# Kernel tuning notes

Measured on AMD Instinct MI355X. Metric: run time of the kernel, lower is better.

## Reference

```python
import jax, jax.numpy as jnp
import numpy as np

NUM_HEADS = 16
HEAD_DIM = 128
EMBED_DIM = 2048
BASE = 10000.0


def rope(x, offset=0):
    # x: [b, h, n, d]  rotary positional embedding (lrpe_type=1)
    d = x.shape[-1]
    n = x.shape[-2]
    inv_freq = 1.0 / (BASE ** (jnp.arange(0, d, 2, dtype=jnp.float32) / d))  # [d/2]
    pos = jnp.arange(n, dtype=jnp.float32) + offset                          # [n]
    ang = pos[:, None] * inv_freq[None, :]                                   # [n, d/2]
    cos, sin = jnp.cos(ang), jnp.sin(ang)
    x1, x2 = x[..., 0::2], x[..., 1::2]
    out1 = x1 * cos - x2 * sin
    out2 = x1 * sin + x2 * cos
    return jnp.stack([out1, out2], axis=-1).reshape(x.shape)


def setup_inputs() -> dict:
    key = jax.random.key(0)
    ks = jax.random.split(key, 5)
    b, n = 2, 2048
    std = 0.02
    x = jax.random.normal(ks[0], (b, n, EMBED_DIM), dtype=jnp.float32)
    Wq = jax.random.normal(ks[1], (NUM_HEADS * HEAD_DIM, EMBED_DIM), dtype=jnp.float32) * std
    Wkv = jax.random.normal(ks[2], (2 * HEAD_DIM, EMBED_DIM), dtype=jnp.float32) * std
    Wkvh = jax.random.normal(ks[3], (2 * NUM_HEADS, EMBED_DIM), dtype=jnp.float32) * std
    Wo = jax.random.normal(ks[4], (EMBED_DIM, NUM_HEADS * HEAD_DIM), dtype=jnp.float32) * std
    return {"x": x, "Wq": Wq, "Wkv": Wkv, "Wkvh": Wkvh, "Wo": Wo}


def reference(x, Wq, Wkv, Wkvh, Wo):
    b, n, _ = x.shape
    h, d = NUM_HEADS, HEAD_DIM
    q = x @ Wq.T                     # [b, n, h*d]
    kv = x @ Wkv.T                   # [b, n, 2d]
    kvh = x @ Wkvh.T                 # [b, n, 2h]  (mpa_activation='none')
    k, v = kv[..., :d], kv[..., d:]
    k_head, v_head = kvh[..., :h], kvh[..., h:]
    # gate_type=0: per-token outer product broadcast of the single kv to all heads
    k = jnp.einsum('bnd,bnh->bhnd', k, k_head)
    v = jnp.einsum('bnd,bnh->bhnd', v, v_head)
    q = q.reshape(b, n, h, d).transpose(0, 2, 1, 3)  # [b, h, n, d]
    q = rope(q)
    k = rope(k)
    scale = 1.0 / jnp.sqrt(jnp.float32(d))
    scores = jnp.einsum('bhqd,bhkd->bhqk', q, k) * scale
    causal = jnp.tril(jnp.ones((n, n), dtype=bool))
    scores = jnp.where(causal, scores, -jnp.inf)
    attn = jax.nn.softmax(scores, axis=-1)
    o = jnp.einsum('bhqk,bhkd->bhqd', attn, v)
    o = o.transpose(0, 2, 1, 3).reshape(b, n, h * d)
    return o @ Wo.T
```

## Files before the change

kernel.cpp:

```cpp
#include <hip/hip_runtime.h>
#include <stdint.h>

#define BB 2
#define HH 16
#define NN 2048
#define DD 128
#define EE 2048

typedef short s16x8 __attribute__((ext_vector_type(8)));
typedef float fx4 __attribute__((ext_vector_type(4)));

static __device__ __forceinline__ unsigned short f2bf(float f) {
  unsigned u = __builtin_bit_cast(unsigned, f);
  u += 0x7fffu + ((u >> 16) & 1u);
  return (unsigned short)(u >> 16);
}
static __device__ __forceinline__ float bf2f(unsigned short h) {
  unsigned u = ((unsigned)h) << 16;
  return __builtin_bit_cast(float, u);
}
static __device__ __forceinline__ void gload_lds16(const void* g, void* l) {
  __builtin_amdgcn_global_load_lds(
      (const __attribute__((address_space(1))) unsigned int*)g,
      (__attribute__((address_space(3))) unsigned int*)l, 16, 0, 0);
}
static __device__ __forceinline__ unsigned cvt_pk_bf16(float lo, float hi) {
  unsigned w;
  asm("v_cvt_pk_bf16_f32 %0, %1, %2" : "=v"(w) : "v"(lo), "v"(hi));
  return w;
}

__global__ __launch_bounds__(256) void f2b_kernel(const float* __restrict__ in,
                                                  unsigned short* __restrict__ out,
                                                  int n4) {
  int i = blockIdx.x * 256 + threadIdx.x;
  if (i < n4) {
    float4 v = ((const float4*)in)[i];
    uint2 o;
    o.x = ((unsigned)f2bf(v.y) << 16) | f2bf(v.x);
    o.y = ((unsigned)f2bf(v.w) << 16) | f2bf(v.z);
    ((uint2*)out)[i] = o;
  }
}

#define GBK 64

#define GEMM_STAGE(LDSB, SRCBASE, rowb)                                        \
  _Pragma("unroll") for (int t = 0; t < 4; ++t) {                              \
    int r = wave * 32 + t * 8 + (lane >> 3);                                   \
    int ch = (lane & 7) ^ (r & 7);                                             \
    const unsigned char* src = (SRCBASE) + (size_t)r * (rowb) + ch * 16;       \
    gload_lds16(src, (void*)((LDSB) + (wave * 32 + t * 8) * 128));             \
  }

#define GEMM_LOOP_BODY                                                         \
  for (int k0 = 0; k0 < K; k0 += GBK) {                                        \
    const unsigned char* ag = Ag + (size_t)k0 * 2;                             \
    const unsigned char* bg = Bg + (size_t)k0 * 2;                             \
    __syncthreads();                                                           \
    GEMM_STAGE(Alds, ag, rowb)                                                 \
    GEMM_STAGE(Blds, bg, rowb)                                                 \
    __syncthreads();                                                           \
    _Pragma("unroll") for (int kk = 0; kk < 2; ++kk) {                         \
      s16x8 af[4], bf[4];                                                      \
      _Pragma("unroll") for (int i = 0; i < 4; ++i) {                          \
        int row = wr * 64 + i * 16 + lr;                                       \
        int chunk = (kk * 4 + g) ^ (row & 7);                                  \
        af[i] = *(const s16x8*)(Alds + row * 128 + chunk * 16);                \
      }                                                                        \
      _Pragma("unroll") for (int j = 0; j < 4; ++j) {                          \
        int row = wc * 64 + j * 16 + lr;                                       \
        int chunk = (kk * 4 + g) ^ (row & 7);                                  \
        bf[j] = *(const s16x8*)(Blds + row * 128 + chunk * 16);                \
      }                                                                        \
      _Pragma("unroll") for (int i = 0; i < 4; ++i)                            \
        _Pragma("unroll") for (int j = 0; j < 4; ++j)                          \
          acc[i][j] = __builtin_amdgcn_mfma_f32_16x16x32_bf16(af[i], bf[j],    \
                                                              acc[i][j], 0, 0, 0); \
    }                                                                          \
  }

#define GEMM_PROLOG                                                            \
  __shared__ alignas(16) unsigned char Alds[128 * 128];                        \
  __shared__ alignas(16) unsigned char Blds[128 * 128];                        \
  const int tid = threadIdx.x;                                                 \
  const int wave = tid >> 6, lane = tid & 63;                                  \
  const int g = lane >> 4, lr = lane & 15;                                     \
  const int mtiles = M / 128;                                                  \
  const int mt = blockIdx.x % mtiles, nt = blockIdx.x / mtiles;                \
  const int m0 = mt * 128, n0 = nt * 128;                                      \
  const int wr = wave >> 1, wc = wave & 1;                                     \
  fx4 acc[4][4];                                                               \
  _Pragma("unroll") for (int i = 0; i < 4; ++i)                                \
    _Pragma("unroll") for (int j = 0; j < 4; ++j)                              \
      acc[i][j] = (fx4){0.f, 0.f, 0.f, 0.f};                                   \
  const unsigned char* Ag = (const unsigned char*)(A + (size_t)m0 * K);        \
  const unsigned char* Bg = (const unsigned char*)(B + (size_t)n0 * K);        \
  const size_t rowb = (size_t)K * 2;

__global__ __launch_bounds__(256) void gemm_out(const unsigned short* __restrict__ A,
                                                const unsigned short* __restrict__ B,
                                                float* __restrict__ Cf,
                                                int M, int N, int K) {
  GEMM_PROLOG
  GEMM_LOOP_BODY
#pragma unroll
  for (int i = 0; i < 4; ++i) {
    int row = m0 + wr * 64 + i * 16 + 4 * g;
#pragma unroll
    for (int j = 0; j < 4; ++j) {
      int col = n0 + wc * 64 + j * 16 + lr;
#pragma unroll
      for (int r = 0; r < 4; ++r)
        Cf[(size_t)(row + r) * N + col] = acc[i][j][r];
    }
  }
}

__global__ __launch_bounds__(256) void gemm_qkv(const unsigned short* __restrict__ A,
                                                const unsigned short* __restrict__ B,
                                                unsigned short* __restrict__ qrope,
                                                unsigned short* __restrict__ kvb,
                                                int M, int N, int K) {
  GEMM_PROLOG
  GEMM_LOOP_BODY
#pragma unroll
  for (int j = 0; j < 4; ++j) {
    int col = n0 + wc * 64 + j * 16 + lr;
    if (col < 2048) {
      int hh = col >> 7, d = col & 127;
      float invf = __expf(-0.14391156831212787f * (float)(d >> 1));
      int par = d & 1;
#pragma unroll
      for (int i = 0; i < 4; ++i) {
#pragma unroll
        for (int r = 0; r < 4; ++r) {
          int row = m0 + wr * 64 + i * 16 + 4 * g + r;
          int n = row & (NN - 1), bq = row >> 11;
          float self = acc[i][j][r];
          float other = __shfl_xor(self, 1);
          float sn, cs;
          __sincosf((float)n * invf, &sn, &cs);
          float a = self * cs, bt = other * sn;
          float o = par ? (a + bt) : (a - bt);
          qrope[((size_t)(bq * HH + hh) * NN + n) * DD + d] = f2bf(o);
        }
      }
    } else {
      int c2 = col - 2048;
#pragma unroll
      for (int i = 0; i < 4; ++i) {
#pragma unroll
        for (int r = 0; r < 4; ++r) {
          int row = m0 + wr * 64 + i * 16 + 4 * g + r;
          kvb[(size_t)row * 256 + c2] = f2bf(acc[i][j][r]);
        }
      }
    }
  }
}

__global__ __launch_bounds__(256) void kvh_mfma(const unsigned short* __restrict__ X,
                                                const unsigned short* __restrict__ Wb,
                                                float* __restrict__ out) {
  const int tid = threadIdx.x;
  const int wave = tid >> 6, lane = tid & 63;
  const int g = lane >> 4, lr = lane & 15;
  const int rowbase = blockIdx.x * 32 + (wave & 1) * 16;
  const int colbase = (wave >> 1) * 16;

  const unsigned short* xr = X + (size_t)(rowbase + lr) * EE + 8 * g;
  const unsigned short* wr = Wb + (size_t)(colbase + lr) * EE + 8 * g;

  fx4 acc = (fx4){0.f, 0.f, 0.f, 0.f};
#pragma unroll 8
  for (int k0 = 0; k0 < EE; k0 += 32) {
    s16x8 a = *(const s16x8*)(xr + k0);
    s16x8 b = *(const s16x8*)(wr + k0);
    acc = __builtin_amdgcn_mfma_f32_16x16x32_bf16(a, b, acc, 0, 0, 0);
  }
  const int j = colbase + lr;
  const int head = j & 15, sel = j >> 4;
#pragma unroll
  for (int r = 0; r < 4; ++r) {
    int m = rowbase + 4 * g + r;
    int b = m >> 11, n = m & (NN - 1);
    out[(((size_t)(b * HH + head)) * NN + n) * 2 + sel] = acc[r];
  }
}

__global__ __launch_bounds__(256) void rope_k(const unsigned short* __restrict__ kv,
                                              unsigned short* __restrict__ ko) {
  int idx = blockIdx.x * 256 + threadIdx.x;
  int i = idx & 63;
  int bn = idx >> 6;
  int n = bn & (NN - 1);
  unsigned v = *(const unsigned*)(kv + (size_t)bn * 256 + 2 * i);
  float x1 = bf2f((unsigned short)(v & 0xffff));
  float x2 = bf2f((unsigned short)(v >> 16));
  float inv = __expf(-0.14391156831212787f * (float)i);
  float ang = (float)n * inv;
  float sn, cs;
  __sincosf(ang, &sn, &cs);
  float o1 = x1 * cs - x2 * sn, o2 = x1 * sn + x2 * cs;
  unsigned ov = ((unsigned)f2bf(o2) << 16) | f2bf(o1);
  *(unsigned*)(ko + (size_t)bn * DD + 2 * i) = ov;
}

__global__ __launch_bounds__(256) void vtrans(const unsigned short* __restrict__ kv,
                                              unsigned short* __restrict__ vT) {
  __shared__ unsigned short t[64][40];
  int bx = blockIdx.x;
  int b = bx >> 7;
  int d0 = ((bx >> 5) & 3) * 32;
  int n0 = (bx & 31) * 64;
  int tid = threadIdx.x;
  {
    int i = tid >> 2;
    int c = (tid & 3) * 8;
    s16x8 v = *(const s16x8*)(kv + ((size_t)(b * NN + n0 + i)) * 256 + 128 + d0 + c);
#pragma unroll
    for (int u = 0; u < 8; ++u) t[i][c + u] = (unsigned short)v[u];
  }
  __syncthreads();
  {
    int j = tid >> 3;
    int cc = (tid & 7) * 8;
    s16x8 o;
#pragma unroll
    for (int u = 0; u < 8; ++u) o[u] = (short)t[cc + u][j];
    *(s16x8*)(vT + ((size_t)(b * DD + d0 + j)) * NN + n0 + cc) = o;
  }
}

#define QB 128
#define KB 64

__global__ __launch_bounds__(512, 2) void attn(const unsigned short* __restrict__ Q,
                                               const unsigned short* __restrict__ Kr,
                                               const unsigned short* __restrict__ VT,
                                               const float* __restrict__ KVHP,
                                               unsigned short* __restrict__ O) {
  __shared__ alignas(16) unsigned char Klds[2 * 64 * 256];
  __shared__ alignas(16) unsigned char Vlds[2 * 128 * 128];
  __shared__ alignas(16) unsigned char Plds[16 * 16 * 128];
  __shared__ float2 mlbuf[4][2][16];

  const int qp = blockIdx.x;
  const int h = blockIdx.y;
  const int b = blockIdx.z;
  const int tid = threadIdx.x;
  const int wave = tid >> 6, lane = tid & 63;
  const int parity = wave >> 2, wq = wave & 3;
  const int g = lane >> 4, lr = lane & 15;
  const size_t bh = (size_t)(b * HH + h);

  const float scale2 = 0.08838834764831845f * 1.4426950408889634f;
  const unsigned short* Kb = Kr + (size_t)b * NN * DD;
  const unsigned short* VTb = VT + (size_t)b * DD * NN;
  const float2* KVp = (const float2*)KVHP + (size_t)(b * HH + h) * NN;

  unsigned char* Kl = Klds + parity * (64 * 256);
  unsigned char* Vl = Vlds + parity * (128 * 128);
  float* Obuf = (float*)Plds;

  auto STAGE = [&](int key0s) {
#pragma unroll
    for (int j = 0; j < 4; ++j) {
      int rl = wq * 16 + j * 4 + (lane >> 4);
      int ch = (lane & 15) ^ (rl & 7);
      const unsigned char* gp = (const unsigned char*)(Kb + (size_t)(key0s + rl) * DD) + ch * 16;
      gload_lds16(gp, (void*)(Kl + (wq * 16 + j * 4) * 256));
    }
#pragma unroll
    for (int j = 0; j < 4; ++j) {
      int row = wq * 32 + j * 8 + (lane >> 3);
      int c = lane & 7;
      const unsigned short* gp = VTb + (size_t)row * NN + key0s + ((c ^ (row & 7)) * 8);
      gload_lds16(gp, (void*)(Vl + (wq * 32 + j * 8) * 128));
    }
  };

  auto PHASE = [&](int qt) {
    const int qbase_w = qt * QB + wq * 32;

    s16x8 qf[2][4];
#pragma unroll
    for (int qq = 0; qq < 2; ++qq) {
      const unsigned short* qptr = Q + (bh * NN + qbase_w + qq * 16 + lr) * DD + 8 * g;
#pragma unroll
      for (int dc = 0; dc < 4; ++dc) qf[qq][dc] = *(const s16x8*)(qptr + dc * 32);
    }

    float m_run[2] = {-1e30f, -1e30f}, l_run[2] = {0.f, 0.f};
    fx4 oacc[2][8];
#pragma unroll
    for (int qq = 0; qq < 2; ++qq)
#pragma unroll
      for (int d = 0; d < 8; ++d) oacc[qq][d] = (fx4){0.f, 0.f, 0.f, 0.f};

    const int cnt = qt + 1;
    for (int i = 0; i < cnt; ++i) {
      const int key0 = (2 * i + parity) * KB;
      __syncthreads();
      fx4 khv[4], vhv[4];
#pragma unroll
      for (int kb = 0; kb < 4; ++kb) {
        const float4* kp = (const float4*)(KVp + key0 + kb * 16 + 4 * g);
        float4 f0 = kp[0];
        float4 f1 = kp[1];
        khv[kb] = (fx4){f0.x * scale2, f0.z * scale2, f1.x * scale2, f1.z * scale2};
        vhv[kb] = (fx4){f0.y, f0.w, f1.y, f1.w};
      }
      STAGE(key0);
      __syncthreads();

      if (key0 <= qbase_w + 31) {
        fx4 sacc[2][4];
#pragma unroll
        for (int qq = 0; qq < 2; ++qq)
#pragma unroll
          for (int kb = 0; kb < 4; ++kb) sacc[qq][kb] = (fx4){0.f, 0.f, 0.f, 0.f};
        __builtin_amdgcn_s_setprio(1);
#pragma unroll
        for (int kb = 0; kb < 4; ++kb) {
#pragma unroll
          for (int dc = 0; dc < 4; ++dc) {
            int key = kb * 16 + lr;
            int chunk = (dc * 4 + g) ^ (key & 7);
            s16x8 kf = *(const s16x8*)(Kl + key * 256 + chunk * 16);
            sacc[0][kb] = __builtin_amdgcn_mfma_f32_16x16x32_bf16(kf, qf[0][dc], sacc[0][kb], 0, 0, 0);
            sacc[1][kb] = __builtin_amdgcn_mfma_f32_16x16x32_bf16(kf, qf[1][dc], sacc[1][kb], 0, 0, 0);
          }
        }
        __builtin_amdgcn_s_setprio(0);

#pragma unroll
        for (int qq = 0; qq < 2; ++qq) {
          const int qg = qbase_w + qq * 16 + lr;
          float smax = -1e30f;
          if (key0 + 63 > qbase_w + qq * 16) {
#pragma unroll
            for (int kb = 0; kb < 4; ++kb) {
#pragma unroll
              for (int r = 0; r < 4; ++r) {
                int keyg = key0 + kb * 16 + 4 * g + r;
                float s = sacc[qq][kb][r] * khv[kb][r];
                if (keyg > qg) s = -1e30f;
                sacc[qq][kb][r] = s;
                smax = fmaxf(smax, s);
              }
            }
          } else {
#pragma unroll
            for (int kb = 0; kb < 4; ++kb) {
#pragma unroll
              for (int r = 0; r < 4; ++r) {
                float s = sacc[qq][kb][r] * khv[kb][r];
                sacc[qq][kb][r] = s;
                smax = fmaxf(smax, s);
              }
            }
          }
          smax = fmaxf(smax, __shfl_xor(smax, 16));
          smax = fmaxf(smax, __shfl_xor(smax, 32));
          if (!__all(smax - m_run[qq] <= 8.0f)) {
            float mnew = fmaxf(m_run[qq], smax);
            float corr = exp2f(m_run[qq] - mnew);
            m_run[qq] = mnew;
            l_run[qq] *= corr;
            float cr[4];
#pragma unroll
            for (int r = 0; r < 4; ++r) cr[r] = __shfl(corr, 4 * g + r);
#pragma unroll
            for (int d = 0; d < 8; ++d)
#pragma unroll
              for (int r = 0; r < 4; ++r) oacc[qq][d][r] *= cr[r];
          }
          float rsum = 0.f;
#pragma unroll
          for (int kb = 0; kb < 4; ++kb) {
            float p0 = exp2f(sacc[qq][kb][0] - m_run[qq]);
            float p1 = exp2f(sacc[qq][kb][1] - m_run[qq]);
            float p2 = exp2f(sacc[qq][kb][2] - m_run[qq]);
            float p3 = exp2f(sacc[qq][kb][3] - m_run[qq]);
            rsum += (p0 + p1) + (p2 + p3);
            uint2 w;
            w.x = cvt_pk_bf16(p0 * vhv[kb][0], p1 * vhv[kb][1]);
            w.y = cvt_pk_bf16(p2 * vhv[kb][2], p3 * vhv[kb][3]);
            int chunk = (kb * 2 + (g >> 1)) ^ (lr & 7);
            *(uint2*)(Plds + (wave * 2 + qq) * 2048 + lr * 128 + chunk * 16 + (g & 1) * 8) = w;
          }
          rsum += __shfl_xor(rsum, 16);
          rsum += __shfl_xor(rsum, 32);
          l_run[qq] += rsum;
        }

        s16x8 pa[2][2];
#pragma unroll
        for (int qq = 0; qq < 2; ++qq)
#pragma unroll
          for (int kk = 0; kk < 2; ++kk) {
            int chunk = (kk * 4 + g) ^ (lr & 7);
            pa[qq][kk] = *(const s16x8*)(Plds + (wave * 2 + qq) * 2048 + lr * 128 + chunk * 16);
          }
        __builtin_amdgcn_s_setprio(1);
#pragma unroll
        for (int dc = 0; dc < 8; ++dc) {
#pragma unroll
          for (int kk = 0; kk < 2; ++kk) {
            int d = dc * 16 + lr;
            int chunk = (kk * 4 + g) ^ (d & 7);
            s16x8 vf = *(const s16x8*)(Vl + d * 128 + chunk * 16);
            oacc[0][dc] = __builtin_amdgcn_mfma_f32_16x16x32_bf16(pa[0][kk], vf, oacc[0][dc], 0, 0, 0);
            oacc[1][dc] = __builtin_amdgcn_mfma_f32_16x16x32_bf16(pa[1][kk], vf, oacc[1][dc], 0, 0, 0);
          }
        }
        __builtin_amdgcn_s_setprio(0);
      }
    }

    __syncthreads();
    if (parity == 1 && g == 0) {
#pragma unroll
      for (int qq = 0; qq < 2; ++qq)
        mlbuf[wq][qq][lr] = make_float2(m_run[qq], l_run[qq]);
    }
    __syncthreads();
    float lC[2], af0[2][4], af1[2][4];
    if (parity == 0) {
#pragma unroll
      for (int qq = 0; qq < 2; ++qq) {
        float2 ml1 = mlbuf[wq][qq][lr];
        float M = fmaxf(m_run[qq], ml1.x);
        float a0 = exp2f(m_run[qq] - M);
        float a1 = exp2f(ml1.x - M);
        lC[qq] = l_run[qq] * a0 + ml1.y * a1;
#pragma unroll
        for (int r = 0; r < 4; ++r) {
          af0[qq][r] = __shfl(a0, 4 * g + r);
          af1[qq][r] = __shfl(a1, 4 * g + r);
        }
      }
    }
#pragma unroll
    for (int dh = 0; dh < 2; ++dh) {
      if (parity == 1) {
#pragma unroll
        for (int qq = 0; qq < 2; ++qq)
#pragma unroll
          for (int dc2 = 0; dc2 < 4; ++dc2)
#pragma unroll
            for (int r = 0; r < 4; ++r)
              Obuf[wq * 2048 + (qq * 16 + 4 * g + r) * 64 + dc2 * 16 + lr] =
                  oacc[qq][dh * 4 + dc2][r];
      }
      __syncthreads();
      if (parity == 0) {
#pragma unroll
        for (int qq = 0; qq < 2; ++qq)
#pragma unroll
          for (int dc2 = 0; dc2 < 4; ++dc2)
#pragma unroll
            for (int r = 0; r < 4; ++r) {
              float o1 = Obuf[wq * 2048 + (qq * 16 + 4 * g + r) * 64 + dc2 * 16 + lr];
              oacc[qq][dh * 4 + dc2][r] =
                  oacc[qq][dh * 4 + dc2][r] * af0[qq][r] + o1 * af1[qq][r];
            }
      }
      __syncthreads();
    }
    if (parity == 0) {
#pragma unroll
      for (int qq = 0; qq < 2; ++qq) {
        float inv = 1.0f / lC[qq];
#pragma unroll
        for (int r = 0; r < 4; ++r) {
          float invr = __shfl(inv, 4 * g + r);
          int qout = qbase_w + qq * 16 + 4 * g + r;
          unsigned short* orow = O + (((size_t)b * NN + qout) * HH + h) * DD;
#pragma unroll
          for (int dc = 0; dc < 8; ++dc) orow[dc * 16 + lr] = f2bf(oacc[qq][dc][r] * invr);
        }
      }
    }
  };

  PHASE(qp);
  PHASE(15 - qp);
}

extern "C" void kernel_launch(void* const* d_in, const int* in_sizes, int n_in,
                              void* d_out, int out_size, void* d_ws, size_t ws_size,
                              hipStream_t stream) {
  const float* x = (const float*)d_in[0];
  const float* Wq = (const float*)d_in[1];
  const float* Wkv = (const float*)d_in[2];
  const float* Wkvh = (const float*)d_in[3];
  const float* Wo = (const float*)d_in[4];
  float* out = (float*)d_out;
  char* ws = (char*)d_ws;

  unsigned short* xb    = (unsigned short*)(ws + 0);
  unsigned short* obuf  = xb;
  unsigned short* wqkv  = (unsigned short*)(ws + 16777216);
  unsigned short* vtb   = wqkv;
  unsigned short* wob   = (unsigned short*)(ws + 26214400);
  unsigned short* kvb   = (unsigned short*)(ws + 34603008);
  unsigned short* wkvhb = (unsigned short*)(ws + 53477376);
  float*          kvhb  = (float*)(ws + 53608448);
  unsigned short* qrope = (unsigned short*)(ws + 54132736);
  unsigned short* krope = (unsigned short*)(ws + 70909952);

  f2b_kernel<<<8192, 256, 0, stream>>>(x, xb, 2097152);
  f2b_kernel<<<4096, 256, 0, stream>>>(Wq, wqkv, 1048576);
  f2b_kernel<<<512, 256, 0, stream>>>(Wkv, wqkv + 4194304, 131072);
  f2b_kernel<<<4096, 256, 0, stream>>>(Wo, wob, 1048576);
  f2b_kernel<<<64, 256, 0, stream>>>(Wkvh, wkvhb, 16384);

  gemm_qkv<<<576, 256, 0, stream>>>(xb, wqkv, qrope, kvb, 4096, 2304, 2048);
  kvh_mfma<<<128, 256, 0, stream>>>(xb, wkvhb, kvhb);

  rope_k<<<1024, 256, 0, stream>>>(kvb, krope);
  vtrans<<<256, 256, 0, stream>>>(kvb, vtb);

  dim3 ag(8, HH, BB);
  attn<<<ag, 512, 0, stream>>>(qrope, krope, vtb, kvhb, obuf);

  gemm_out<<<512, 256, 0, stream>>>(obuf, wob, out, 4096, 2048, 2048);
}
```

Measured before the change: 221.0 us.

## Fuse K rope and V transpose into QKV GEMM epilogue; merge conversion launches

The QKV GEMM epilogue now branches on column tile: Q tiles apply rope as before, the K tile applies rope in-register and writes krope directly, and V tiles write transposed bf16 V straight into the vT layout. This removes the separate rope_k and vtrans kernels and the kvb intermediate round trip through memory. The five fp32-to-bf16 conversion launches are merged into one kernel that picks its source by block index, cutting launch overhead. The V epilogue writes 8-byte strided chunks into the transposed layout, which may coalesce less well than the old transpose kernel.

```diff
diff --git a/kernel.cpp b/kernel.cpp
--- a/kernel.cpp
+++ b/kernel.cpp
@@ -30,17 +30,29 @@
   return w;
 }
 
-__global__ __launch_bounds__(256) void f2b_kernel(const float* __restrict__ in,
-                                                  unsigned short* __restrict__ out,
-                                                  int n4) {
-  int i = blockIdx.x * 256 + threadIdx.x;
-  if (i < n4) {
-    float4 v = ((const float4*)in)[i];
-    uint2 o;
-    o.x = ((unsigned)f2bf(v.y) << 16) | f2bf(v.x);
-    o.y = ((unsigned)f2bf(v.w) << 16) | f2bf(v.z);
-    ((uint2*)out)[i] = o;
-  }
+__global__ __launch_bounds__(256) void f2b_all(const float* __restrict__ x,
+                                               const float* __restrict__ Wq,
+                                               const float* __restrict__ Wkv,
+                                               const float* __restrict__ Wo,
+                                               const float* __restrict__ Wkvh,
+                                               unsigned short* __restrict__ xb,
+                                               unsigned short* __restrict__ wqkv,
+                                               unsigned short* __restrict__ wob,
+                                               unsigned short* __restrict__ wkvhb) {
+  int bid = blockIdx.x;
+  const float* in;
+  unsigned short* out;
+  int i;
+  if (bid < 8192) { in = x; out = xb; i = bid * 256 + threadIdx.x; }
+  else if (bid < 12288) { in = Wq; out = wqkv; i = (bid - 8192) * 256 + threadIdx.x; }
+  else if (bid < 12800) { in = Wkv; out = wqkv + 4194304; i = (bid - 12288) * 256 + threadIdx.x; }
+  else if (bid < 16896) { in = Wo; out = wob; i = (bid - 12800) * 256 + threadIdx.x; }
+  else { in = Wkvh; out = wkvhb; i = (bid - 16896) * 256 + threadIdx.x; }
+  float4 v = ((const float4*)in)[i];
+  uint2 o;
+  o.x = ((unsigned)f2bf(v.y) << 16) | f2bf(v.x);
+  o.y = ((unsigned)f2bf(v.w) << 16) | f2bf(v.z);
+  ((uint2*)out)[i] = o;
 }
 
 #define GBK 64
@@ -120,14 +132,15 @@
 __global__ __launch_bounds__(256) void gemm_qkv(const unsigned short* __restrict__ A,
                                                 const unsigned short* __restrict__ B,
                                                 unsigned short* __restrict__ qrope,
-                                                unsigned short* __restrict__ kvb,
+                                                unsigned short* __restrict__ krope,
+                                                unsigned short* __restrict__ vT,
                                                 int M, int N, int K) {
   GEMM_PROLOG
   GEMM_LOOP_BODY
-#pragma unroll
-  for (int j = 0; j < 4; ++j) {
-    int col = n0 + wc * 64 + j * 16 + lr;
-    if (col < 2048) {
+  if (nt < 16) {
+#pragma unroll
+    for (int j = 0; j < 4; ++j) {
+      int col = n0 + wc * 64 + j * 16 + lr;
       int hh = col >> 7, d = col & 127;
       float invf = __expf(-0.14391156831212787f * (float)(d >> 1));
       int par = d & 1;
@@ -146,15 +159,43 @@
           qrope[((size_t)(bq * HH + hh) * NN + n) * DD + d] = f2bf(o);
         }
       }
-    } else {
-      int c2 = col - 2048;
+    }
+  } else if (nt == 16) {
+#pragma unroll
+    for (int j = 0; j < 4; ++j) {
+      int col = n0 + wc * 64 + j * 16 + lr;
+      int d = col - 2048;
+      float invf = __expf(-0.14391156831212787f * (float)(d >> 1));
+      int par = d & 1;
 #pragma unroll
       for (int i = 0; i < 4; ++i) {
 #pragma unroll
         for (int r = 0; r < 4; ++r) {
           int row = m0 + wr * 64 + i * 16 + 4 * g + r;
-          kvb[(size_t)row * 256 + c2] = f2bf(acc[i][j][r]);
-        }
+          int n = row & (NN - 1);
+          float self = acc[i][j][r];
+          float other = __shfl_xor(self, 1);
+          float sn, cs;
+          __sincosf((float)n * invf, &sn, &cs);
+          float a = self * cs, bt = other * sn;
+          float o = par ? (a + bt) : (a - bt);
+          krope[(size_t)row * DD + d] = f2bf(o);
+        }
+      }
+    }
+  } else {
+#pragma unroll
+    for (int j = 0; j < 4; ++j) {
+      int col = n0 + wc * 64 + j * 16 + lr;
+      int d = col - 2176;
+#pragma unroll
+      for (int i = 0; i < 4; ++i) {
+        int nbase = m0 + wr * 64 + i * 16 + 4 * g;
+        int bq = nbase >> 11, n = nbase & (NN - 1);
+        uint2 w;
+        w.x = cvt_pk_bf16(acc[i][j][0], acc[i][j][1]);
+        w.y = cvt_pk_bf16(acc[i][j][2], acc[i][j][3]);
+        *(uint2*)(vT + ((size_t)(bq * DD + d)) * NN + n) = w;
       }
     }
   }
@@ -186,50 +227,6 @@
     int m = rowbase + 4 * g + r;
     int b = m >> 11, n = m & (NN - 1);
     out[(((size_t)(b * HH + head)) * NN + n) * 2 + sel] = acc[r];
-  }
-}
-
-__global__ __launch_bounds__(256) void rope_k(const unsigned short* __restrict__ kv,
-                                              unsigned short* __restrict__ ko) {
-  int idx = blockIdx.x * 256 + threadIdx.x;
-  int i = idx & 63;
-  int bn = idx >> 6;
-  int n = bn & (NN - 1);
-  unsigned v = *(const unsigned*)(kv + (size_t)bn * 256 + 2 * i);
-  float x1 = bf2f((unsigned short)(v & 0xffff));
-  float x2 = bf2f((unsigned short)(v >> 16));
-  float inv = __expf(-0.14391156831212787f * (float)i);
-  float ang = (float)n * inv;
-  float sn, cs;
-  __sincosf(ang, &sn, &cs);
-  float o1 = x1 * cs - x2 * sn, o2 = x1 * sn + x2 * cs;
-  unsigned ov = ((unsigned)f2bf(o2) << 16) | f2bf(o1);
-  *(unsigned*)(ko + (size_t)bn * DD + 2 * i) = ov;
-}
-
-__global__ __launch_bounds__(256) void vtrans(const unsigned short* __restrict__ kv,
-                                              unsigned short* __restrict__ vT) {
-  __shared__ unsigned short t[64][40];
-  int bx = blockIdx.x;
-  int b = bx >> 7;
-  int d0 = ((bx >> 5) & 3) * 32;
-  int n0 = (bx & 31) * 64;
-  int tid = threadIdx.x;
-  {
-    int i = tid >> 2;
-    int c = (tid & 3) * 8;
-    s16x8 v = *(const s16x8*)(kv + ((size_t)(b * NN + n0 + i)) * 256 + 128 + d0 + c);
-#pragma unroll
-    for (int u = 0; u < 8; ++u) t[i][c + u] = (unsigned short)v[u];
-  }
-  __syncthreads();
-  {
-    int j = tid >> 3;
-    int cc = (tid & 7) * 8;
-    s16x8 o;
-#pragma unroll
-    for (int u = 0; u < 8; ++u) o[u] = (short)t[cc + u][j];
-    *(s16x8*)(vT + ((size_t)(b * DD + d0 + j)) * NN + n0 + cc) = o;
   }
 }
 
@@ -504,25 +501,17 @@
   unsigned short* xb    = (unsigned short*)(ws + 0);
   unsigned short* obuf  = xb;
   unsigned short* wqkv  = (unsigned short*)(ws + 16777216);
-  unsigned short* vtb   = wqkv;
   unsigned short* wob   = (unsigned short*)(ws + 26214400);
-  unsigned short* kvb   = (unsigned short*)(ws + 34603008);
+  unsigned short* vtb   = (unsigned short*)(ws + 34603008);
   unsigned short* wkvhb = (unsigned short*)(ws + 53477376);
   float*          kvhb  = (float*)(ws + 53608448);
   unsigned short* qrope = (unsigned short*)(ws + 54132736);
   unsigned short* krope = (unsigned short*)(ws + 70909952);
 
-  f2b_kernel<<<8192, 256, 0, stream>>>(x, xb, 2097152);
-  f2b_kernel<<<4096, 256, 0, stream>>>(Wq, wqkv, 1048576);
-  f2b_kernel<<<512, 256, 0, stream>>>(Wkv, wqkv + 4194304, 131072);
-  f2b_kernel<<<4096, 256, 0, stream>>>(Wo, wob, 1048576);
-  f2b_kernel<<<64, 256, 0, stream>>>(Wkvh, wkvhb, 16384);
-
-  gemm_qkv<<<576, 256, 0, stream>>>(xb, wqkv, qrope, kvb, 4096, 2304, 2048);
+  f2b_all<<<16960, 256, 0, stream>>>(x, Wq, Wkv, Wo, Wkvh, xb, wqkv, wob, wkvhb);
+
+  gemm_qkv<<<576, 256, 0, stream>>>(xb, wqkv, qrope, krope, vtb, 4096, 2304, 2048);
   kvh_mfma<<<128, 256, 0, stream>>>(xb, wkvhb, kvhb);
-
-  rope_k<<<1024, 256, 0, stream>>>(kvb, krope);
-  vtrans<<<256, 256, 0, stream>>>(kvb, vtb);
 
   dim3 ag(8, HH, BB);
   attn<<<ag, 512, 0, stream>>>(qrope, krope, vtb, kvhb, obuf);
```

Result: slower. 235.1 us (+6.4%).

## Register-prefetch next K/V tile in attention and fuse fp32-to-bf16 conversion launches

Applied to the files above, without the earlier changes.

The attention loop now loads the next K/V tile from global memory into registers while the current tile is being computed, then writes it to LDS at the start of the next iteration. This replaces the direct global-to-LDS loads that were issued and waited on before each compute step, so the load latency is meant to overlap with the MFMA work. The five separate fp32-to-bf16 conversion launches are also merged into one kernel that picks its source by block index, cutting launch overhead. The V-transpose buffer moves to its own workspace region so it no longer aliases the weight buffer. The costs are higher register pressure from holding the prefetched tile and an extra barrier per iteration.

```diff
diff --git a/kernel.cpp b/kernel.cpp
--- a/kernel.cpp
+++ b/kernel.cpp
@@ -30,17 +30,29 @@
   return w;
 }
 
-__global__ __launch_bounds__(256) void f2b_kernel(const float* __restrict__ in,
-                                                  unsigned short* __restrict__ out,
-                                                  int n4) {
-  int i = blockIdx.x * 256 + threadIdx.x;
-  if (i < n4) {
-    float4 v = ((const float4*)in)[i];
-    uint2 o;
-    o.x = ((unsigned)f2bf(v.y) << 16) | f2bf(v.x);
-    o.y = ((unsigned)f2bf(v.w) << 16) | f2bf(v.z);
-    ((uint2*)out)[i] = o;
-  }
+__global__ __launch_bounds__(256) void f2b_all(const float* __restrict__ x,
+                                               const float* __restrict__ Wq,
+                                               const float* __restrict__ Wkv,
+                                               const float* __restrict__ Wo,
+                                               const float* __restrict__ Wkvh,
+                                               unsigned short* __restrict__ xb,
+                                               unsigned short* __restrict__ wqkv,
+                                               unsigned short* __restrict__ wob,
+                                               unsigned short* __restrict__ wkvhb) {
+  int bid = blockIdx.x;
+  const float* in;
+  unsigned short* out;
+  int i;
+  if (bid < 8192) { in = x; out = xb; i = bid * 256 + threadIdx.x; }
+  else if (bid < 12288) { in = Wq; out = wqkv; i = (bid - 8192) * 256 + threadIdx.x; }
+  else if (bid < 12800) { in = Wkv; out = wqkv + 4194304; i = (bid - 12288) * 256 + threadIdx.x; }
+  else if (bid < 16896) { in = Wo; out = wob; i = (bid - 12800) * 256 + threadIdx.x; }
+  else { in = Wkvh; out = wkvhb; i = (bid - 16896) * 256 + threadIdx.x; }
+  float4 v = ((const float4*)in)[i];
+  uint2 o;
+  o.x = ((unsigned)f2bf(v.y) << 16) | f2bf(v.x);
+  o.y = ((unsigned)f2bf(v.w) << 16) | f2bf(v.z);
+  ((uint2*)out)[i] = o;
 }
 
 #define GBK 64
@@ -264,21 +276,28 @@
   unsigned char* Vl = Vlds + parity * (128 * 128);
   float* Obuf = (float*)Plds;
 
-  auto STAGE = [&](int key0s) {
+  s16x8 kreg[4], vreg[4];
+  auto LOADREGS = [&](int key0s) {
 #pragma unroll
     for (int j = 0; j < 4; ++j) {
       int rl = wq * 16 + j * 4 + (lane >> 4);
       int ch = (lane & 15) ^ (rl & 7);
-      const unsigned char* gp = (const unsigned char*)(Kb + (size_t)(key0s + rl) * DD) + ch * 16;
-      gload_lds16(gp, (void*)(Kl + (wq * 16 + j * 4) * 256));
+      kreg[j] = *(const s16x8*)((const unsigned char*)(Kb + (size_t)(key0s + rl) * DD) + ch * 16);
     }
 #pragma unroll
     for (int j = 0; j < 4; ++j) {
       int row = wq * 32 + j * 8 + (lane >> 3);
       int c = lane & 7;
-      const unsigned short* gp = VTb + (size_t)row * NN + key0s + ((c ^ (row & 7)) * 8);
-      gload_lds16(gp, (void*)(Vl + (wq * 32 + j * 8) * 128));
-    }
+      vreg[j] = *(const s16x8*)(VTb + (size_t)row * NN + key0s + ((c ^ (row & 7)) * 8));
+    }
+  };
+  auto WRITELDS = [&]() {
+#pragma unroll
+    for (int j = 0; j < 4; ++j)
+      *(s16x8*)(Kl + (wq * 16 + j * 4) * 256 + lane * 16) = kreg[j];
+#pragma unroll
+    for (int j = 0; j < 4; ++j)
+      *(s16x8*)(Vl + (wq * 32 + j * 8) * 128 + lane * 16) = vreg[j];
   };
 
   auto PHASE = [&](int qt) {
@@ -300,9 +319,16 @@
       for (int d = 0; d < 8; ++d) oacc[qq][d] = (fx4){0.f, 0.f, 0.f, 0.f};
 
     const int cnt = qt + 1;
+    LOADREGS(parity * KB);
+
     for (int i = 0; i < cnt; ++i) {
       const int key0 = (2 * i + parity) * KB;
       __syncthreads();
+      WRITELDS();
+      __syncthreads();
+
+      if (i + 1 < cnt) LOADREGS(key0 + 2 * KB);
+
       fx4 khv[4], vhv[4];
 #pragma unroll
       for (int kb = 0; kb < 4; ++kb) {
@@ -312,8 +338,6 @@
         khv[kb] = (fx4){f0.x * scale2, f0.z * scale2, f1.x * scale2, f1.z * scale2};
         vhv[kb] = (fx4){f0.y, f0.w, f1.y, f1.w};
       }
-      STAGE(key0);
-      __syncthreads();
 
       if (key0 <= qbase_w + 31) {
         fx4 sacc[2][4];
@@ -504,19 +528,15 @@
   unsigned short* xb    = (unsigned short*)(ws + 0);
   unsigned short* obuf  = xb;
   unsigned short* wqkv  = (unsigned short*)(ws + 16777216);
-  unsigned short* vtb   = wqkv;
   unsigned short* wob   = (unsigned short*)(ws + 26214400);
   unsigned short* kvb   = (unsigned short*)(ws + 34603008);
+  unsigned short* vtb   = (unsigned short*)(ws + 36700160);
   unsigned short* wkvhb = (unsigned short*)(ws + 53477376);
   float*          kvhb  = (float*)(ws + 53608448);
   unsigned short* qrope = (unsigned short*)(ws + 54132736);
   unsigned short* krope = (unsigned short*)(ws + 70909952);
 
-  f2b_kernel<<<8192, 256, 0, stream>>>(x, xb, 2097152);
-  f2b_kernel<<<4096, 256, 0, stream>>>(Wq, wqkv, 1048576);
-  f2b_kernel<<<512, 256, 0, stream>>>(Wkv, wqkv + 4194304, 131072);
-  f2b_kernel<<<4096, 256, 0, stream>>>(Wo, wob, 1048576);
-  f2b_kernel<<<64, 256, 0, stream>>>(Wkvh, wkvhb, 16384);
+  f2b_all<<<16960, 256, 0, stream>>>(x, Wq, Wkv, Wo, Wkvh, xb, wqkv, wob, wkvhb);
 
   gemm_qkv<<<576, 256, 0, stream>>>(xb, wqkv, qrope, kvb, 4096, 2304, 2048);
   kvh_mfma<<<128, 256, 0, stream>>>(xb, wkvhb, kvhb);
```

Measured after the change: 239.2 us. +8.3%, slower.
